# Optimization experiments

Measured on AMD Instinct MI355X. Metric: run time of the kernel, lower is better.

The kernel has to match this reference:

```python
import jax, jax.numpy as jnp
import numpy as np

TINY = 1e-6
MIN_DEG, MAX_DEG = 0, 16

# 3x21 icosahedral basis used for the background (non-diag) IPE
P = jnp.asarray(np.array([
    0.8506508, 0.0, 0.5257311, 0.809017, 0.5, 0.309017, 0.5257311, 0.8506508, 0.0,
    1.0, 0.0, 0.0, 0.809017, 0.5, -0.309017, 0.8506508, 0.0, -0.5257311, 0.309017,
    0.809017, -0.5, 0.0, 0.5257311, -0.8506508, 0.5, 0.309017, -0.809017, 0.0, 1.0,
    0.0, -0.5257311, 0.8506508, 0.0, -0.309017, 0.809017, -0.5, 0.0, 0.5257311,
    0.8506508, -0.309017, 0.809017, 0.5, 0.309017, 0.809017, 0.5, 0.5, 0.309017,
    0.809017, 0.5, -0.309017, 0.809017, 0.0, 0.0, 1.0, -0.5, 0.309017, 0.809017,
    -0.809017, 0.5, 0.309017, -0.809017, 0.5, -0.309017], dtype=np.float32).reshape(3, 21))


def setup_inputs() -> dict:
    key = jax.random.key(0)
    k1, k2, k3, k4, k5 = jax.random.split(key, 5)
    N, Ns = 2048, 64
    ray_o = jax.random.normal(k1, (N, 3), dtype=jnp.float32)
    ray_d = jax.random.normal(k2, (N, 3), dtype=jnp.float32)
    fg_z_vals = jnp.sort(jax.random.uniform(k3, (N, Ns + 1), minval=0.1, maxval=5.0), axis=-1)
    bg_z_vals = jnp.sort(jax.random.uniform(k4, (N, Ns + 1), minval=1.0, maxval=50.0), axis=-1)
    radii = jax.random.uniform(k5, (N, 1), minval=0.005, maxval=0.02)
    return {"ray_o": ray_o, "ray_d": ray_d, "fg_z_vals": fg_z_vals,
            "bg_z_vals": bg_z_vals, "radii": radii}


def _frustum_moments(t0, t1, base_radius):
    mu = (t0 + t1) / 2.0
    hw = (t1 - t0) / 2.0
    denom = 3.0 * mu ** 2 + hw ** 2
    t_mean = mu + 2.0 * mu * hw ** 2 / denom
    t_var = hw ** 2 / 3.0 - (4.0 / 15.0) * (hw ** 4 * (12.0 * mu ** 2 - hw ** 2) / denom ** 2)
    r_var = base_radius ** 2 * (mu ** 2 / 4.0 + (5.0 / 12.0) * hw ** 2 - (4.0 / 15.0) * hw ** 4 / denom)
    return t_mean, t_var, r_var


def cast_rays_diag(t_vals, origins, directions, radii):
    t_mean, t_var, r_var = _frustum_moments(t_vals[..., :-1], t_vals[..., 1:], radii)
    d = directions[..., None, :]                      # [N,1,3]
    mean = d * t_mean[..., None]                      # [N,Ns,3]
    d_mag_sq = jnp.maximum(1e-8, jnp.sum(d ** 2, axis=-1, keepdims=True))
    d_outer_diag = d ** 2
    null_outer_diag = 1.0 - d_outer_diag / d_mag_sq
    cov_diag = t_var[..., None] * d_outer_diag + r_var[..., None] * null_outer_diag
    return mean + origins[..., None, :], cov_diag


def cast_rays_full(t_vals, origins, directions, radii):
    t_mean, t_var, r_var = _frustum_moments(t_vals[..., :-1], t_vals[..., 1:], radii)
    d = directions[..., None, :]                      # [N,1,3]
    mean = d * t_mean[..., None]                      # [N,Ns,3]
    d_mag_sq = jnp.maximum(1e-8, jnp.sum(d ** 2, axis=-1, keepdims=True))
    d_outer = d[..., :, None] * d[..., None, :]       # [N,1,3,3]
    eye = jnp.eye(3, dtype=d.dtype)
    null_outer = eye - d[..., :, None] * (d / d_mag_sq)[..., None, :]
    cov = t_var[..., None, None] * d_outer + r_var[..., None, None] * null_outer
    return mean + origins[..., None, :], cov          # [N,Ns,3], [N,Ns,3,3]


def _contract_point(x):
    n = jnp.linalg.norm(x) + TINY
    return (2.0 - 1.0 / n) * (x / n)


def contract_gaussian(mean, cov_full):
    N, Ns = mean.shape[0], mean.shape[1]
    flat = mean.reshape(-1, 3)
    J = jax.vmap(jax.jacfwd(_contract_point))(flat).reshape(N, Ns, 3, 3)
    n = jnp.linalg.norm(mean, axis=-1, keepdims=True) + TINY
    mean_c = (2.0 - 1.0 / n) * (mean / n)
    cov_c = jnp.einsum('nsij,nsjk,nslk->nsil', J, cov_full, J)
    return mean_c, cov_c


def expected_sin(x, x_var):
    return jnp.exp(-0.5 * x_var) * jnp.sin(x)


def ipe_diag(x, x_cov_diag, min_deg, max_deg):
    scales = 2.0 ** jnp.arange(min_deg, max_deg, dtype=x.dtype)   # [L]
    N, Ns = x.shape[0], x.shape[1]
    y = (x[..., None, :] * scales[:, None]).reshape(N, Ns, -1)                 # [N,Ns,L*3]
    y_var = (x_cov_diag[..., None, :] * (scales ** 2)[:, None]).reshape(N, Ns, -1)
    return expected_sin(jnp.concatenate([y, y + 0.5 * jnp.pi], axis=-1),
                        jnp.concatenate([y_var, y_var], axis=-1))


def ipe_full(x, x_cov, min_deg, max_deg):
    y = jnp.matmul(x, P)                                                        # [N,Ns,21]
    y_var = jnp.einsum('nsab,bk,ak->nsk', x_cov, P, P)                          # [N,Ns,21]
    scales = 2.0 ** jnp.arange(min_deg, max_deg, dtype=x.dtype)
    N, Ns = x.shape[0], x.shape[1]
    y = (y[..., None, :] * scales[:, None]).reshape(N, Ns, -1)                  # [N,Ns,L*21]
    y_var = (y_var[..., None, :] * (scales ** 2)[:, None]).reshape(N, Ns, -1)
    return expected_sin(jnp.concatenate([y, y + 0.5 * jnp.pi], axis=-1),
                        jnp.concatenate([y_var, y_var], axis=-1))


def reference(ray_o, ray_d, fg_z_vals, bg_z_vals, radii):
    # foreground: diagonal-cov cone cast + diagonal IPE  -> [N,Ns,96]
    fg_mean, fg_cov_diag = cast_rays_diag(fg_z_vals, ray_o, ray_d, radii)
    enc_fg = ipe_diag(fg_mean, fg_cov_diag, MIN_DEG, MAX_DEG)
    # background: full-cov cone cast + contraction Jacobian + basis IPE -> [N,Ns,672]
    bg_mean, bg_cov = cast_rays_full(bg_z_vals, ray_o, ray_d, radii)
    mean_c, cov_c = contract_gaussian(bg_mean, bg_cov)
    enc_bg = ipe_full(mean_c, cov_c, MIN_DEG, MAX_DEG)
    return jnp.concatenate([enc_fg, enc_bg], axis=-1)                            # [N,Ns,768]
```

## Files before the change

### kernel.cpp

```cpp
#include <hip/hip_runtime.h>
#include <math.h>

#define NS 64
#define INV2PI  0.15915494309189535f
#define NEGHL2E (-0.72134752044448170f)

typedef __attribute__((ext_vector_type(4))) float vfloat4;

__constant__ float c_P[63] = {
  0.8506508f, 0.0f, 0.5257311f, 0.809017f, 0.5f, 0.309017f, 0.5257311f,
  0.8506508f, 0.0f, 1.0f, 0.0f, 0.0f, 0.809017f, 0.5f, -0.309017f,
  0.8506508f, 0.0f, -0.5257311f, 0.309017f, 0.809017f, -0.5f,
  0.0f, 0.5257311f, -0.8506508f, 0.5f, 0.309017f, -0.809017f, 0.0f, 1.0f,
  0.0f, -0.5257311f, 0.8506508f, 0.0f, -0.309017f, 0.809017f, -0.5f, 0.0f,
  0.5257311f, 0.8506508f, -0.309017f, 0.809017f, 0.5f,
  0.309017f, 0.809017f, 0.5f, 0.5f, 0.309017f, 0.809017f, 0.5f, -0.309017f,
  0.809017f, 0.0f, 0.0f, 1.0f, -0.5f, 0.309017f, 0.809017f, -0.809017f,
  0.5f, 0.309017f, -0.809017f, 0.5f, -0.309017f
};

struct Moments { float t_mean, t_var, r_var; };

__device__ inline Moments frustum_moments(float t0, float t1, float radius) {
    float mu  = 0.5f * (t0 + t1);
    float hw  = 0.5f * (t1 - t0);
    float mu2 = mu * mu, hw2 = hw * hw;
    float denom = 3.0f * mu2 + hw2;
    float inv_d = 1.0f / denom;
    float hw4 = hw2 * hw2;
    Moments m;
    m.t_mean = mu + 2.0f * mu * hw2 * inv_d;
    m.t_var  = hw2 * (1.0f / 3.0f)
             - (4.0f / 15.0f) * (hw4 * (12.0f * mu2 - hw2) * inv_d * inv_d);
    m.r_var  = radius * radius *
               (0.25f * mu2 + (5.0f / 12.0f) * hw2 - (4.0f / 15.0f) * hw4 * inv_d);
    return m;
}

__global__ __launch_bounds__(256, 4) void mipnerf_enc(
    const float* __restrict__ ray_o,
    const float* __restrict__ ray_d,
    const float* __restrict__ fgz,
    const float* __restrict__ bgz,
    const float* __restrict__ radii,
    float* __restrict__ out)
{
    const int n   = blockIdx.x;
    const int tid = threadIdx.x;

    __shared__ float sXV[NS * 50];
    __shared__ float sCore[NS * 11];
    __shared__ unsigned int sDesc[384];

    const float ox = ray_o[3 * n + 0], oy = ray_o[3 * n + 1], oz = ray_o[3 * n + 2];
    const float dx = ray_d[3 * n + 0], dy = ray_d[3 * n + 1], dz = ray_d[3 * n + 2];
    const float rad = radii[n];
    const float dm = fmaxf(1e-8f, dx * dx + dy * dy + dz * dz);
    const float inv_dm = 1.0f / dm;

    if (tid < NS) {
        const int s = tid;
        {
            float t0 = fgz[(NS + 1) * n + s];
            float t1 = fgz[(NS + 1) * n + s + 1];
            Moments mm = frustum_moments(t0, t1, rad);
            float d3[3] = {dx, dy, dz};
            float o3[3] = {ox, oy, oz};
            #pragma unroll
            for (int i = 0; i < 3; ++i) {
                float m  = o3[i] + d3[i] * mm.t_mean;
                float dd = d3[i] * d3[i];
                float cd = mm.t_var * dd + mm.r_var * (1.0f - dd * inv_dm);
                sXV[s * 50 + 2 * (21 + i) + 0] = m  * INV2PI;
                sXV[s * 50 + 2 * (21 + i) + 1] = cd * NEGHL2E;
            }
        }
        {
            float t0 = bgz[(NS + 1) * n + s];
            float t1 = bgz[(NS + 1) * n + s + 1];
            Moments mm = frustum_moments(t0, t1, rad);
            float x0 = ox + dx * mm.t_mean;
            float x1 = oy + dy * mm.t_mean;
            float x2 = oz + dz * mm.t_mean;
            float a  = mm.t_var - mm.r_var * inv_dm;
            float rv = mm.r_var;
            float rn2 = x0 * x0 + x1 * x1 + x2 * x2;
            float rn  = sqrtf(rn2);
            float nn  = rn + 1e-6f;
            float inn = 1.0f / nn;
            float g   = (2.0f * nn - 1.0f) * inn * inn;
            float gp  = 2.0f * (1.0f - nn) * inn * inn * inn;
            float h   = gp / rn;
            float xd  = x0 * dx + x1 * dy + x2 * dz;
            float hxd = h * xd;
            float u0 = g * dx + hxd * x0;
            float u1 = g * dy + hxd * x1;
            float u2 = g * dz + hxd * x2;
            float w  = 2.0f * g * h + h * h * rn2;
            float* cr = &sCore[s * 11];
            cr[0] = x0; cr[1] = x1; cr[2] = x2;
            cr[3] = u0; cr[4] = u1; cr[5] = u2;
            cr[6] = g;  cr[7] = a;  cr[8] = rv * g * g; cr[9] = rv * w;
        }
    } else {
        for (int e = tid - NS; e < 384; e += 256 - NS) {
            int deg, src;
            if (e < 48) { deg = e / 3;  src = 21 + (e - 3 * deg); }
            else { int jj = e - 48; deg = jj / 21; src = jj - 21 * deg; }
            sDesc[e] = ((unsigned)(127 + deg) << 23) | ((unsigned)src << 3);
        }
    }
    __syncthreads();

    #pragma unroll
    for (int j = 0; j < 6; ++j) {
        int i = tid + 256 * j;
        if (i < 21 * NS) {
            int k = i >> 6;
            int s = i & (NS - 1);
            const float p0 = c_P[k], p1 = c_P[21 + k], p2 = c_P[42 + k];
            const float* cr = &sCore[s * 11];
            float x0 = cr[0], x1 = cr[1], x2 = cr[2];
            float u0 = cr[3], u1 = cr[4], u2 = cr[5];
            float g = cr[6], c1 = cr[7], c2 = cr[8], c3 = cr[9];
            float dpx = p0 * x0 + p1 * x1 + p2 * x2;
            float dpu = p0 * u0 + p1 * u1 + p2 * u2;
            float pp  = p0 * p0 + p1 * p1 + p2 * p2;
            float y   = g * dpx;
            float yv  = c1 * dpu * dpu + c2 * pp + c3 * dpx * dpx;
            sXV[s * 50 + 2 * k + 0] = y  * INV2PI;
            sXV[s * 50 + 2 * k + 1] = yv * NEGHL2E;
        }
    }
    __syncthreads();

    float* __restrict__ outp = out + (size_t)n * (NS * 768);

    for (int it = 0; it < 24; ++it) {
        int p  = tid + 256 * it;
        int s  = p / 96;
        int j0 = (p - s * 96) << 2;
        const uint4 w4 = *reinterpret_cast<const uint4*>(&sDesc[j0]);
        const char* rowXV = reinterpret_cast<const char*>(&sXV[s * 50]);
        const bool fg = (j0 < 48);

        vfloat4 vs, vc;
        {
            unsigned w = w4.x;
            float sf = __uint_as_float(w & 0xFF800000u);
            float2 xv = *reinterpret_cast<const float2*>(rowXV + (w & 0xFFu));
            float e  = __builtin_amdgcn_exp2f(xv.y * (sf * sf));
            float xs = xv.x * sf;
            vs.x = e * __builtin_amdgcn_sinf(__builtin_amdgcn_fractf(xs));
            vc.x = e * __builtin_amdgcn_sinf(__builtin_amdgcn_fractf(xs + 0.25f));
        }
        {
            unsigned w = w4.y;
            float sf = __uint_as_float(w & 0xFF800000u);
            float2 xv = *reinterpret_cast<const float2*>(rowXV + (w & 0xFFu));
            float e  = __builtin_amdgcn_exp2f(xv.y * (sf * sf));
            float xs = xv.x * sf;
            vs.y = e * __builtin_amdgcn_sinf(__builtin_amdgcn_fractf(xs));
            vc.y = e * __builtin_amdgcn_sinf(__builtin_amdgcn_fractf(xs + 0.25f));
        }
        {
            unsigned w = w4.z;
            float sf = __uint_as_float(w & 0xFF800000u);
            float2 xv = *reinterpret_cast<const float2*>(rowXV + (w & 0xFFu));
            float e  = __builtin_amdgcn_exp2f(xv.y * (sf * sf));
            float xs = xv.x * sf;
            vs.z = e * __builtin_amdgcn_sinf(__builtin_amdgcn_fractf(xs));
            vc.z = e * __builtin_amdgcn_sinf(__builtin_amdgcn_fractf(xs + 0.25f));
        }
        {
            unsigned w = w4.w;
            float sf = __uint_as_float(w & 0xFF800000u);
            float2 xv = *reinterpret_cast<const float2*>(rowXV + (w & 0xFFu));
            float e  = __builtin_amdgcn_exp2f(xv.y * (sf * sf));
            float xs = xv.x * sf;
            vs.w = e * __builtin_amdgcn_sinf(__builtin_amdgcn_fractf(xs));
            vc.w = e * __builtin_amdgcn_sinf(__builtin_amdgcn_fractf(xs + 0.25f));
        }

        float* o1 = outp + (s * 768 + (fg ? j0 : j0 + 48));
        float* o2 = o1 + (fg ? 48 : 336);
        __builtin_nontemporal_store(vs, reinterpret_cast<vfloat4*>(o1));
        __builtin_nontemporal_store(vc, reinterpret_cast<vfloat4*>(o2));
    }
}

extern "C" void kernel_launch(void* const* d_in, const int* in_sizes, int n_in,
                              void* d_out, int out_size, void* d_ws, size_t ws_size,
                              hipStream_t stream) {
    const float* ray_o = (const float*)d_in[0];
    const float* ray_d = (const float*)d_in[1];
    const float* fgz   = (const float*)d_in[2];
    const float* bgz   = (const float*)d_in[3];
    const float* radii = (const float*)d_in[4];
    float* out = (float*)d_out;
    const int N = in_sizes[0] / 3;
    mipnerf_enc<<<N, 256, 0, stream>>>(ray_o, ray_d, fgz, bgz, radii, out);
}
```

Measured before the change: 416.9 us.

## Split encoder into per-sample prep kernel and emit kernel via workspace

Splits the fused kernel in two. A prep kernel runs one thread per (ray, sample) and writes 24 float2 (scaled mean, log-variance) entries to a global workspace. An emit kernel reads these entries and writes the sin/cos outputs, using a compile-time descriptor table in constant memory instead of building it in shared memory. This removes the serial per-ray setup phase, the shared-memory staging and the two block barriers, at the cost of an extra launch and a round trip of about 25 MB through global memory. The fused kernel is kept as a fallback when no workspace is available.

```diff
diff --git a/kernel.cpp b/kernel.cpp
--- a/kernel.cpp
+++ b/kernel.cpp
@@ -18,6 +18,19 @@
   0.809017f, 0.0f, 0.0f, 1.0f, -0.5f, 0.309017f, 0.809017f, -0.809017f,
   0.5f, 0.309017f, -0.809017f, 0.5f, -0.309017f
 };
+
+struct DescTab { unsigned v[384]; };
+static constexpr DescTab make_desc() {
+    DescTab t{};
+    for (int e = 0; e < 384; ++e) {
+        int deg, src;
+        if (e < 48) { deg = e / 3;  src = 21 + (e - 3 * deg); }
+        else        { int jj = e - 48; deg = jj / 21; src = jj - 21 * deg; }
+        t.v[e] = ((unsigned)(127 + deg) << 23) | ((unsigned)src << 3);
+    }
+    return t;
+}
+__constant__ DescTab cDesc = make_desc();
 
 struct Moments { float t_mean, t_var, r_var; };
 
@@ -35,6 +48,139 @@
     m.r_var  = radius * radius *
                (0.25f * mu2 + (5.0f / 12.0f) * hw2 - (4.0f / 15.0f) * hw4 * inv_d);
     return m;
+}
+
+__global__ __launch_bounds__(256) void mipnerf_prep(
+    const float* __restrict__ ray_o,
+    const float* __restrict__ ray_d,
+    const float* __restrict__ fgz,
+    const float* __restrict__ bgz,
+    const float* __restrict__ radii,
+    float2* __restrict__ ws)
+{
+    const int idx = blockIdx.x * 256 + threadIdx.x;
+    const int n = idx >> 6;
+    const int s = idx & (NS - 1);
+
+    const float ox = ray_o[3 * n + 0], oy = ray_o[3 * n + 1], oz = ray_o[3 * n + 2];
+    const float dx = ray_d[3 * n + 0], dy = ray_d[3 * n + 1], dz = ray_d[3 * n + 2];
+    const float rad = radii[n];
+    const float dm = fmaxf(1e-8f, dx * dx + dy * dy + dz * dz);
+    const float inv_dm = 1.0f / dm;
+
+    float2* __restrict__ row = ws + (size_t)idx * 24;
+
+    {
+        float t0 = fgz[(NS + 1) * n + s];
+        float t1 = fgz[(NS + 1) * n + s + 1];
+        Moments mm = frustum_moments(t0, t1, rad);
+        float d3[3] = {dx, dy, dz};
+        float o3[3] = {ox, oy, oz};
+        #pragma unroll
+        for (int i = 0; i < 3; ++i) {
+            float m  = o3[i] + d3[i] * mm.t_mean;
+            float dd = d3[i] * d3[i];
+            float cd = mm.t_var * dd + mm.r_var * (1.0f - dd * inv_dm);
+            row[21 + i] = make_float2(m * INV2PI, cd * NEGHL2E);
+        }
+    }
+    {
+        float t0 = bgz[(NS + 1) * n + s];
+        float t1 = bgz[(NS + 1) * n + s + 1];
+        Moments mm = frustum_moments(t0, t1, rad);
+        float x0 = ox + dx * mm.t_mean;
+        float x1 = oy + dy * mm.t_mean;
+        float x2 = oz + dz * mm.t_mean;
+        float a  = mm.t_var - mm.r_var * inv_dm;
+        float rv = mm.r_var;
+        float rn2 = x0 * x0 + x1 * x1 + x2 * x2;
+        float rn  = sqrtf(rn2);
+        float nn  = rn + 1e-6f;
+        float inn = 1.0f / nn;
+        float g   = (2.0f * nn - 1.0f) * inn * inn;
+        float gp  = 2.0f * (1.0f - nn) * inn * inn * inn;
+        float h   = gp / rn;
+        float xd  = x0 * dx + x1 * dy + x2 * dz;
+        float hxd = h * xd;
+        float u0 = g * dx + hxd * x0;
+        float u1 = g * dy + hxd * x1;
+        float u2 = g * dz + hxd * x2;
+        float w  = 2.0f * g * h + h * h * rn2;
+        float c1 = a, c2 = rv * g * g, c3 = rv * w;
+        #pragma unroll
+        for (int k = 0; k < 21; ++k) {
+            const float p0 = c_P[k], p1 = c_P[21 + k], p2 = c_P[42 + k];
+            float dpx = p0 * x0 + p1 * x1 + p2 * x2;
+            float dpu = p0 * u0 + p1 * u1 + p2 * u2;
+            float pp  = p0 * p0 + p1 * p1 + p2 * p2;
+            float y   = g * dpx;
+            float yv  = c1 * dpu * dpu + c2 * pp + c3 * dpx * dpx;
+            row[k] = make_float2(y * INV2PI, yv * NEGHL2E);
+        }
+    }
+}
+
+__global__ __launch_bounds__(256, 4) void mipnerf_emit(
+    const float2* __restrict__ ws,
+    float* __restrict__ out)
+{
+    const int n   = blockIdx.x;
+    const int tid = threadIdx.x;
+    const char* __restrict__ wbase = reinterpret_cast<const char*>(ws + (size_t)n * (NS * 24));
+    float* __restrict__ outp = out + (size_t)n * (NS * 768);
+    const unsigned* dtab = cDesc.v;
+
+    for (int it = 0; it < 24; ++it) {
+        int p  = it * 256 + tid;
+        int s  = p / 96;
+        int j0 = (p - s * 96) << 2;
+        const uint4 w4 = *reinterpret_cast<const uint4*>(&dtab[j0]);
+        const char* rowXV = wbase + s * 192;
+        const bool fg = (j0 < 48);
+
+        vfloat4 vs, vc;
+        {
+            unsigned w = w4.x;
+            float sf = __uint_as_float(w & 0xFF800000u);
+            float2 xv = *reinterpret_cast<const float2*>(rowXV + (w & 0xFFu));
+            float e  = __builtin_amdgcn_exp2f(xv.y * (sf * sf));
+            float xs = xv.x * sf;
+            vs.x = e * __builtin_amdgcn_sinf(__builtin_amdgcn_fractf(xs));
+            vc.x = e * __builtin_amdgcn_sinf(__builtin_amdgcn_fractf(xs + 0.25f));
+        }
+        {
+            unsigned w = w4.y;
+            float sf = __uint_as_float(w & 0xFF800000u);
+            float2 xv = *reinterpret_cast<const float2*>(rowXV + (w & 0xFFu));
+            float e  = __builtin_amdgcn_exp2f(xv.y * (sf * sf));
+            float xs = xv.x * sf;
+            vs.y = e * __builtin_amdgcn_sinf(__builtin_amdgcn_fractf(xs));
+            vc.y = e * __builtin_amdgcn_sinf(__builtin_amdgcn_fractf(xs + 0.25f));
+        }
+        {
+            unsigned w = w4.z;
+            float sf = __uint_as_float(w & 0xFF800000u);
+            float2 xv = *reinterpret_cast<const float2*>(rowXV + (w & 0xFFu));
+            float e  = __builtin_amdgcn_exp2f(xv.y * (sf * sf));
+            float xs = xv.x * sf;
+            vs.z = e * __builtin_amdgcn_sinf(__builtin_amdgcn_fractf(xs));
+            vc.z = e * __builtin_amdgcn_sinf(__builtin_amdgcn_fractf(xs + 0.25f));
+        }
+        {
+            unsigned w = w4.w;
+            float sf = __uint_as_float(w & 0xFF800000u);
+            float2 xv = *reinterpret_cast<const float2*>(rowXV + (w & 0xFFu));
+            float e  = __builtin_amdgcn_exp2f(xv.y * (sf * sf));
+            float xs = xv.x * sf;
+            vs.w = e * __builtin_amdgcn_sinf(__builtin_amdgcn_fractf(xs));
+            vc.w = e * __builtin_amdgcn_sinf(__builtin_amdgcn_fractf(xs + 0.25f));
+        }
+
+        float* o1 = outp + (s * 768 + (fg ? j0 : j0 + 48));
+        float* o2 = o1 + (fg ? 48 : 336);
+        __builtin_nontemporal_store(vs, reinterpret_cast<vfloat4*>(o1));
+        __builtin_nontemporal_store(vc, reinterpret_cast<vfloat4*>(o2));
+    }
 }
 
 __global__ __launch_bounds__(256, 4) void mipnerf_enc(
@@ -199,5 +345,13 @@
     const float* radii = (const float*)d_in[4];
     float* out = (float*)d_out;
     const int N = in_sizes[0] / 3;
-    mipnerf_enc<<<N, 256, 0, stream>>>(ray_o, ray_d, fgz, bgz, radii, out);
-}
+
+    const size_t need = (size_t)N * NS * 24 * sizeof(float2);
+    if (d_ws != nullptr && ws_size >= need && (N % 4) == 0) {
+        mipnerf_prep<<<(N * NS) / 256, 256, 0, stream>>>(ray_o, ray_d, fgz, bgz, radii,
+                                                         (float2*)d_ws);
+        mipnerf_emit<<<N, 256, 0, stream>>>((const float2*)d_ws, out);
+    } else {
+        mipnerf_enc<<<N, 256, 0, stream>>>(ray_o, ray_d, fgz, bgz, radii, out);
+    }
+}
```

New measurement: 429.5 us. 1.03x slower.

## Restructure output loop so each wave writes contiguous full rows with register-held descriptors

Applied to the files above, without the earlier changes.

Replaces the 384-entry descriptor table with a 768-entry constexpr table that includes a phase bit, so each output column maps directly to its source and phase. Each wave now handles 16 samples and writes whole 768-float rows in three contiguous 1 KB chunks, keeping its three descriptor vectors in registers instead of reloading them from LDS every iteration. This makes the stores fully coalesced and removes the per-iteration index division. In exchange the sin and cos values for an element are no longer shared through a common exp2, so exp2 and the exponent multiply are computed twice as often, and a larger table is copied into LDS.

```diff
diff --git a/kernel.cpp b/kernel.cpp
--- a/kernel.cpp
+++ b/kernel.cpp
@@ -18,6 +18,21 @@
   0.809017f, 0.0f, 0.0f, 1.0f, -0.5f, 0.309017f, 0.809017f, -0.809017f,
   0.5f, 0.309017f, -0.809017f, 0.5f, -0.309017f
 };
+
+struct DescTab768 { unsigned v[768]; };
+static constexpr DescTab768 make_desc768() {
+    DescTab768 t{};
+    for (int c = 0; c < 768; ++c) {
+        int deg, src, ph;
+        if      (c < 48)  { deg = c / 3;               src = 21 + c % 3;        ph = 0; }
+        else if (c < 96)  { int cc = c - 48;  deg = cc / 3;  src = 21 + cc % 3; ph = 1; }
+        else if (c < 432) { int cc = c - 96;  deg = cc / 21; src = cc % 21;     ph = 0; }
+        else              { int cc = c - 432; deg = cc / 21; src = cc % 21;     ph = 1; }
+        t.v[c] = ((unsigned)(127 + deg) << 23) | ((unsigned)src << 3) | (unsigned)ph;
+    }
+    return t;
+}
+__constant__ DescTab768 cDesc = make_desc768();
 
 struct Moments { float t_mean, t_var, r_var; };
 
@@ -37,6 +52,43 @@
     return m;
 }
 
+__device__ inline void emit4(uint4 d, const char* __restrict__ rowXV, float* __restrict__ o) {
+    vfloat4 v;
+    {
+        unsigned wd = d.x;
+        float sf = __uint_as_float(wd & 0xFF800000u);
+        float2 xv = *reinterpret_cast<const float2*>(rowXV + (wd & 0xF8u));
+        float e  = __builtin_amdgcn_exp2f(xv.y * (sf * sf));
+        float ph = (float)(wd & 1u) * 0.25f;
+        v.x = e * __builtin_amdgcn_sinf(__builtin_amdgcn_fractf(xv.x * sf + ph));
+    }
+    {
+        unsigned wd = d.y;
+        float sf = __uint_as_float(wd & 0xFF800000u);
+        float2 xv = *reinterpret_cast<const float2*>(rowXV + (wd & 0xF8u));
+        float e  = __builtin_amdgcn_exp2f(xv.y * (sf * sf));
+        float ph = (float)(wd & 1u) * 0.25f;
+        v.y = e * __builtin_amdgcn_sinf(__builtin_amdgcn_fractf(xv.x * sf + ph));
+    }
+    {
+        unsigned wd = d.z;
+        float sf = __uint_as_float(wd & 0xFF800000u);
+        float2 xv = *reinterpret_cast<const float2*>(rowXV + (wd & 0xF8u));
+        float e  = __builtin_amdgcn_exp2f(xv.y * (sf * sf));
+        float ph = (float)(wd & 1u) * 0.25f;
+        v.z = e * __builtin_amdgcn_sinf(__builtin_amdgcn_fractf(xv.x * sf + ph));
+    }
+    {
+        unsigned wd = d.w;
+        float sf = __uint_as_float(wd & 0xFF800000u);
+        float2 xv = *reinterpret_cast<const float2*>(rowXV + (wd & 0xF8u));
+        float e  = __builtin_amdgcn_exp2f(xv.y * (sf * sf));
+        float ph = (float)(wd & 1u) * 0.25f;
+        v.w = e * __builtin_amdgcn_sinf(__builtin_amdgcn_fractf(xv.x * sf + ph));
+    }
+    __builtin_nontemporal_store(v, reinterpret_cast<vfloat4*>(o));
+}
+
 __global__ __launch_bounds__(256, 4) void mipnerf_enc(
     const float* __restrict__ ray_o,
     const float* __restrict__ ray_d,
@@ -50,7 +102,7 @@
 
     __shared__ float sXV[NS * 50];
     __shared__ float sCore[NS * 11];
-    __shared__ unsigned int sDesc[384];
+    __shared__ __align__(16) unsigned sD[768];
 
     const float ox = ray_o[3 * n + 0], oy = ray_o[3 * n + 1], oz = ray_o[3 * n + 2];
     const float dx = ray_d[3 * n + 0], dy = ray_d[3 * n + 1], dz = ray_d[3 * n + 2];
@@ -103,12 +155,7 @@
             cr[6] = g;  cr[7] = a;  cr[8] = rv * g * g; cr[9] = rv * w;
         }
     } else {
-        for (int e = tid - NS; e < 384; e += 256 - NS) {
-            int deg, src;
-            if (e < 48) { deg = e / 3;  src = 21 + (e - 3 * deg); }
-            else { int jj = e - 48; deg = jj / 21; src = jj - 21 * deg; }
-            sDesc[e] = ((unsigned)(127 + deg) << 23) | ((unsigned)src << 3);
-        }
+        for (int e = tid - NS; e < 768; e += 256 - NS) sD[e] = cDesc.v[e];
     }
     __syncthreads();
 
@@ -134,58 +181,22 @@
     }
     __syncthreads();
 
+    const int lane = tid & 63;
+    const int w    = tid >> 6;
+    const uint4* sD4 = reinterpret_cast<const uint4*>(sD);
+    const uint4 d0 = sD4[lane];
+    const uint4 d1 = sD4[64 + lane];
+    const uint4 d2 = sD4[128 + lane];
+
     float* __restrict__ outp = out + (size_t)n * (NS * 768);
 
-    for (int it = 0; it < 24; ++it) {
-        int p  = tid + 256 * it;
-        int s  = p / 96;
-        int j0 = (p - s * 96) << 2;
-        const uint4 w4 = *reinterpret_cast<const uint4*>(&sDesc[j0]);
+    for (int ss = 0; ss < 16; ++ss) {
+        const int s = w * 16 + ss;
         const char* rowXV = reinterpret_cast<const char*>(&sXV[s * 50]);
-        const bool fg = (j0 < 48);
-
-        vfloat4 vs, vc;
-        {
-            unsigned w = w4.x;
-            float sf = __uint_as_float(w & 0xFF800000u);
-            float2 xv = *reinterpret_cast<const float2*>(rowXV + (w & 0xFFu));
-            float e  = __builtin_amdgcn_exp2f(xv.y * (sf * sf));
-            float xs = xv.x * sf;
-            vs.x = e * __builtin_amdgcn_sinf(__builtin_amdgcn_fractf(xs));
-            vc.x = e * __builtin_amdgcn_sinf(__builtin_amdgcn_fractf(xs + 0.25f));
-        }
-        {
-            unsigned w = w4.y;
-            float sf = __uint_as_float(w & 0xFF800000u);
-            float2 xv = *reinterpret_cast<const float2*>(rowXV + (w & 0xFFu));
-            float e  = __builtin_amdgcn_exp2f(xv.y * (sf * sf));
-            float xs = xv.x * sf;
-            vs.y = e * __builtin_amdgcn_sinf(__builtin_amdgcn_fractf(xs));
-            vc.y = e * __builtin_amdgcn_sinf(__builtin_amdgcn_fractf(xs + 0.25f));
-        }
-        {
-            unsigned w = w4.z;
-            float sf = __uint_as_float(w & 0xFF800000u);
-            float2 xv = *reinterpret_cast<const float2*>(rowXV + (w & 0xFFu));
-            float e  = __builtin_amdgcn_exp2f(xv.y * (sf * sf));
-            float xs = xv.x * sf;
-            vs.z = e * __builtin_amdgcn_sinf(__builtin_amdgcn_fractf(xs));
-            vc.z = e * __builtin_amdgcn_sinf(__builtin_amdgcn_fractf(xs + 0.25f));
-        }
-        {
-            unsigned w = w4.w;
-            float sf = __uint_as_float(w & 0xFF800000u);
-            float2 xv = *reinterpret_cast<const float2*>(rowXV + (w & 0xFFu));
-            float e  = __builtin_amdgcn_exp2f(xv.y * (sf * sf));
-            float xs = xv.x * sf;
-            vs.w = e * __builtin_amdgcn_sinf(__builtin_amdgcn_fractf(xs));
-            vc.w = e * __builtin_amdgcn_sinf(__builtin_amdgcn_fractf(xs + 0.25f));
-        }
-
-        float* o1 = outp + (s * 768 + (fg ? j0 : j0 + 48));
-        float* o2 = o1 + (fg ? 48 : 336);
-        __builtin_nontemporal_store(vs, reinterpret_cast<vfloat4*>(o1));
-        __builtin_nontemporal_store(vc, reinterpret_cast<vfloat4*>(o2));
+        float* orow = outp + s * 768 + lane * 4;
+        emit4(d0, rowXV, orow);
+        emit4(d1, rowXV, orow + 256);
+        emit4(d2, rowXV, orow + 512);
     }
 }
 
```

Result: faster. 406.7 us (-2.5%).
